# Performance work log

Measured on AMD Instinct MI355X. Metric: run time of the kernel, lower is better.

The kernel has to match this reference:

```python
import jax, jax.numpy as jnp
import numpy as np

EPS = 1e-5


def conv1x1(x, w, b):
    # x: [B,C,H,W], w: [O,C], b: [O]
    return jnp.einsum('bchw,oc->bohw', x, w) + b[None, :, None, None]


def adain(content, style):
    # Standard AdaIN: instance-normalize content, re-scale with style's
    # per-channel instance statistics.
    mu_c = content.mean(axis=(2, 3), keepdims=True)
    std_c = jnp.sqrt(content.var(axis=(2, 3), keepdims=True) + EPS)
    mu_s = style.mean(axis=(2, 3), keepdims=True)
    std_s = jnp.sqrt(style.var(axis=(2, 3), keepdims=True) + EPS)
    return std_s * (content - mu_c) / std_c + mu_s


def setup_inputs() -> dict:
    key = jax.random.key(0)
    ks = jax.random.split(key, 12)
    B, C, H, W = 4, 512, 64, 64
    C8 = C // 8
    s_in = 1.0 / np.sqrt(C)
    s_mid = 1.0 / np.sqrt(C8)
    return {
        'x0': jax.random.normal(ks[0], (B, C, H, W), jnp.float32),
        'x1': jax.random.normal(ks[1], (B, C, H, W), jnp.float32),
        'g_w': jax.random.normal(ks[2], (C8, C), jnp.float32) * s_in,
        'g_b': jnp.zeros((C8,), jnp.float32),
        'theta_w': jax.random.normal(ks[3], (C8, C), jnp.float32) * s_in,
        'theta_b': jnp.zeros((C8,), jnp.float32),
        'phi_w': jax.random.normal(ks[4], (C8, C), jnp.float32) * s_in,
        'phi_b': jnp.zeros((C8,), jnp.float32),
        'W_w': jax.random.normal(ks[5], (C, C8), jnp.float32) * s_mid,
        'W_b': jnp.zeros((C,), jnp.float32),
    }


def reference(x0, x1, g_w, g_b, theta_w, theta_b, phi_w, phi_b, W_w, W_b):
    B, C, H, W = x0.shape
    N = H * W
    C8 = C // 8
    g_x = conv1x1(x0, g_w, g_b).reshape(B, C8, N).transpose(0, 2, 1)      # [B,N,C8]
    theta_x = conv1x1(x1, theta_w, theta_b).reshape(B, C8, N)             # [B,C8,N]
    phi_x = conv1x1(x1, phi_w, phi_b).reshape(B, C8, N).transpose(0, 2, 1)  # [B,N,C8]
    f = jnp.einsum('bnc,bcm->bnm', phi_x, theta_x)                        # [B,N,N]
    f_div_C = jax.nn.softmax(f, axis=-1)
    y = jnp.einsum('bnm,bmc->bnc', f_div_C, g_x)                          # [B,N,C8]
    # Faithful to torch .view: reinterpret contiguous [B,N,C8] as [B,C8,H,W]
    y = y.reshape(B, C8, H, W)
    W_y = conv1x1(y, W_w, W_b)                                            # [B,C,H,W]
    return adain(x0, W_y)
```

## Files before the change

kernel.cpp:

```cpp
#include <hip/hip_runtime.h>

#define BB 4
#define CC 512
#define C8 64
#define NN 4096
#define EPSI 1e-5f

typedef unsigned short ushort_t;
typedef unsigned int uint;
typedef __bf16 bf16x8 __attribute__((ext_vector_type(8)));
typedef float f32x4 __attribute__((ext_vector_type(4)));

__device__ inline ushort_t f2bf(float f) {
  uint u = __float_as_uint(f);
  uint r = (u + 0x7FFFu + ((u >> 16) & 1u)) >> 16;
  return (ushort_t)r;
}

__device__ inline bf16x8 ld_bf8(const ushort_t* p) {
  uint4 u = *(const uint4*)p;
  return __builtin_bit_cast(bf16x8, u);
}

__global__ __launch_bounds__(256) void wconv_kernel(
    const float* __restrict__ tw, const float* __restrict__ pw,
    const float* __restrict__ gw, ushort_t* __restrict__ twb,
    ushort_t* __restrict__ pwb, ushort_t* __restrict__ gwb) {
  const int sec = blockIdx.x >> 5;
  const int idx = ((blockIdx.x & 31) * 256 + threadIdx.x) * 4;
  const float* src = sec == 0 ? tw : (sec == 1 ? pw : gw);
  ushort_t* dst = sec == 0 ? twb : (sec == 1 ? pwb : gwb);
  float4 v = *(const float4*)(src + idx);
  uint2 pk;
  pk.x = (uint)f2bf(v.x) | ((uint)f2bf(v.y) << 16);
  pk.y = (uint)f2bf(v.z) | ((uint)f2bf(v.w) << 16);
  *(uint2*)(dst + idx) = pk;
}

__global__ __launch_bounds__(256) void proj2_mfma_kernel(
    const float* __restrict__ x1,
    const ushort_t* __restrict__ twb, const float* __restrict__ tb,
    const ushort_t* __restrict__ pwb, const float* __restrict__ pb,
    ushort_t* __restrict__ thetaT, ushort_t* __restrict__ phiT) {
  __shared__ char xT[32 * 128];
  const int b = blockIdx.y;
  const int n0 = blockIdx.x * 32;
  const int t = threadIdx.x;
  const int l = t & 63;
  const int w = t >> 6;
  const int l15 = l & 15;
  const int lg = l >> 4;
  const int ns = w & 1;
  const int isphi = w >> 1;
  const float* xb = x1 + (size_t)b * CC * NN;
  const ushort_t* wb = isphi ? pwb : twb;
  const float* bias = isphi ? pb : tb;
  ushort_t* outp = isphi ? phiT : thetaT;

  f32x4 acc[4];
#pragma unroll
  for (int s = 0; s < 4; ++s) acc[s] = {0.f, 0.f, 0.f, 0.f};

  const int ldrow = t >> 3;
  const int ldc4 = t & 7;
  const int nfr = ns * 16 + l15;
  const int fchunkbase = nfr * 128;
  for (int k0 = 0; k0 < CC; k0 += 64) {
    __syncthreads();
#pragma unroll
    for (int p = 0; p < 2; ++p) {
      const int kr = ldrow + p * 32;
      float4 v = *(const float4*)(xb + (size_t)(k0 + kr) * NN + n0 + ldc4 * 4);
      ushort_t e0 = f2bf(v.x), e1 = f2bf(v.y), e2 = f2bf(v.z), e3 = f2bf(v.w);
      const int chunk = kr >> 3;
      const int kin = (kr & 7) * 2;
#pragma unroll
      for (int j = 0; j < 4; ++j) {
        const int n = ldc4 * 4 + j;
        ushort_t e = j == 0 ? e0 : (j == 1 ? e1 : (j == 2 ? e2 : e3));
        *(ushort_t*)(xT + n * 128 + (((chunk ^ (n & 7)) << 4) | kin)) = e;
      }
    }
    __syncthreads();
#pragma unroll
    for (int ks = 0; ks < 2; ++ks) {
      bf16x8 bx = *(const bf16x8*)(xT + fchunkbase +
                                   (((ks * 4 + lg) ^ (nfr & 7)) << 4));
#pragma unroll
      for (int rs = 0; rs < 4; ++rs) {
        bf16x8 aw = ld_bf8(wb + (size_t)(rs * 16 + l15) * 512 + k0 + ks * 32 + lg * 8);
        acc[rs] = __builtin_amdgcn_mfma_f32_16x16x32_bf16(aw, bx, acc[rs], 0, 0, 0);
      }
    }
  }
  const size_t nrow = (size_t)b * NN + n0 + ns * 16 + l15;
#pragma unroll
  for (int rs = 0; rs < 4; ++rs) {
    float4 bv = *(const float4*)(bias + rs * 16 + lg * 4);
    float a0 = acc[rs][0] + bv.x;
    float a1 = acc[rs][1] + bv.y;
    float a2 = acc[rs][2] + bv.z;
    float a3 = acc[rs][3] + bv.w;
    uint d0, d1;
    asm("v_cvt_pk_bf16_f32 %0, %1, %2" : "=v"(d0) : "v"(a0), "v"(a1));
    asm("v_cvt_pk_bf16_f32 %0, %1, %2" : "=v"(d1) : "v"(a2), "v"(a3));
    uint2 pk; pk.x = d0; pk.y = d1;
    *(uint2*)(outp + nrow * 64 + rs * 16 + lg * 4) = pk;
  }
}

__global__ __launch_bounds__(256) void proj1_mfma_kernel(
    const float* __restrict__ x0,
    const ushort_t* __restrict__ gwb, const float* __restrict__ gbias,
    ushort_t* __restrict__ g) {
  __shared__ char xT[32 * 128];
  const int b = blockIdx.y;
  const int n0 = blockIdx.x * 32;
  const int t = threadIdx.x;
  const int l = t & 63;
  const int w = t >> 6;
  const int l15 = l & 15;
  const int lg = l >> 4;
  const int ns = w & 1;
  const int rh = w >> 1;
  const float* xb = x0 + (size_t)b * CC * NN;

  f32x4 acc[2];
#pragma unroll
  for (int s = 0; s < 2; ++s) acc[s] = {0.f, 0.f, 0.f, 0.f};

  const int ldrow = t >> 3;
  const int ldc4 = t & 7;
  const int nfr = ns * 16 + l15;
  const int fchunkbase = nfr * 128;
  for (int k0 = 0; k0 < CC; k0 += 64) {
    __syncthreads();
#pragma unroll
    for (int p = 0; p < 2; ++p) {
      const int kr = ldrow + p * 32;
      float4 v = *(const float4*)(xb + (size_t)(k0 + kr) * NN + n0 + ldc4 * 4);
      ushort_t e0 = f2bf(v.x), e1 = f2bf(v.y), e2 = f2bf(v.z), e3 = f2bf(v.w);
      const int chunk = kr >> 3;
      const int kin = (kr & 7) * 2;
#pragma unroll
      for (int j = 0; j < 4; ++j) {
        const int n = ldc4 * 4 + j;
        ushort_t e = j == 0 ? e0 : (j == 1 ? e1 : (j == 2 ? e2 : e3));
        *(ushort_t*)(xT + n * 128 + (((chunk ^ (n & 7)) << 4) | kin)) = e;
      }
    }
    __syncthreads();
#pragma unroll
    for (int ks = 0; ks < 2; ++ks) {
      bf16x8 bx = *(const bf16x8*)(xT + fchunkbase +
                                   (((ks * 4 + lg) ^ (nfr & 7)) << 4));
#pragma unroll
      for (int j = 0; j < 2; ++j) {
        const int rs = rh * 2 + j;
        bf16x8 aw = ld_bf8(gwb + (size_t)(rs * 16 + l15) * 512 + k0 + ks * 32 + lg * 8);
        acc[j] = __builtin_amdgcn_mfma_f32_16x16x32_bf16(aw, bx, acc[j], 0, 0, 0);
      }
    }
  }
  const int ncol = n0 + ns * 16 + l15;
#pragma unroll
  for (int j = 0; j < 2; ++j) {
    const int rbase = (rh * 2 + j) * 16 + lg * 4;
    float4 bv = *(const float4*)(gbias + rbase);
    g[((size_t)b * 64 + rbase + 0) * NN + ncol] = f2bf(acc[j][0] + bv.x);
    g[((size_t)b * 64 + rbase + 1) * NN + ncol] = f2bf(acc[j][1] + bv.y);
    g[((size_t)b * 64 + rbase + 2) * NN + ncol] = f2bf(acc[j][2] + bv.z);
    g[((size_t)b * 64 + rbase + 3) * NN + ncol] = f2bf(acc[j][3] + bv.w);
  }
}

__global__ __launch_bounds__(128) void attn_mfma_kernel(
    const ushort_t* __restrict__ thT,
    const ushort_t* __restrict__ phT,
    const ushort_t* __restrict__ gm,
    float* __restrict__ y) {
  __shared__ char Plds[2][2048];
  const int b = blockIdx.y;
  const int q0 = blockIdx.x * 32;
  const int tid = threadIdx.x;
  const int l = tid & 63;
  const int w = tid >> 6;
  const int l15 = l & 15;
  const int lg = l >> 4;
  const ushort_t* thB = thT + (size_t)b * NN * 64;
  const ushort_t* phB = phT + (size_t)b * NN * 64;
  const ushort_t* gB = gm + (size_t)b * 64 * NN;
  char* Pw = Plds[w];

  bf16x8 qf[2];
  {
    const ushort_t* p = phB + (size_t)(q0 + w * 16 + l15) * 64 + lg * 8;
    qf[0] = ld_bf8(p);
    qf[1] = ld_bf8(p + 32);
  }

  float m_run = -1e30f, l_run = 0.f;
  f32x4 acc[4];
#pragma unroll
  for (int s = 0; s < 4; ++s) acc[s] = {0.f, 0.f, 0.f, 0.f};

  const ushort_t* thL = thB + (size_t)l15 * 64 + lg * 8;
  const ushort_t* gL = gB + (size_t)l15 * 4096 + lg * 8;
  const int pwr = l15 * 128;
  const uint pswz = (uint)((l & 7) << 4);

  for (int m0 = 0; m0 < NN; m0 += 64) {
    f32x4 st[4];
#pragma unroll
    for (int s = 0; s < 4; ++s) st[s] = {0.f, 0.f, 0.f, 0.f};
#pragma unroll
    for (int s = 0; s < 4; ++s) {
      const ushort_t* ts = thL + (size_t)(m0 + 16 * s) * 64;
      bf16x8 a0 = ld_bf8(ts);
      bf16x8 a1 = ld_bf8(ts + 32);
      st[s] = __builtin_amdgcn_mfma_f32_16x16x32_bf16(a0, qf[0], st[s], 0, 0, 0);
      st[s] = __builtin_amdgcn_mfma_f32_16x16x32_bf16(a1, qf[1], st[s], 0, 0, 0);
    }
    bf16x8 ga[4][2];
#pragma unroll
    for (int s = 0; s < 4; ++s) {
      const ushort_t* gs = gL + (size_t)s * 16 * 4096 + m0;
      ga[s][0] = ld_bf8(gs);
      ga[s][1] = ld_bf8(gs + 32);
    }
    float tmax = -1e30f;
#pragma unroll
    for (int s = 0; s < 4; ++s)
#pragma unroll
      for (int r = 0; r < 4; ++r) tmax = fmaxf(tmax, st[s][r]);
    tmax = fmaxf(tmax, __shfl_xor(tmax, 16));
    tmax = fmaxf(tmax, __shfl_xor(tmax, 32));
    const float mn = fmaxf(m_run, tmax);
    const float sc = __expf(m_run - mn);
    float tsum = 0.f;
#pragma unroll
    for (int s = 0; s < 4; ++s)
#pragma unroll
      for (int r = 0; r < 4; ++r) {
        float p = __expf(st[s][r] - mn);
        st[s][r] = p;
        tsum += p;
      }
    tsum += __shfl_xor(tsum, 16);
    tsum += __shfl_xor(tsum, 32);
    l_run = l_run * sc + tsum;
    m_run = mn;
#pragma unroll
    for (int s = 0; s < 4; ++s) acc[s] *= sc;
#pragma unroll
    for (int s = 0; s < 4; ++s) {
      uint d0, d1;
      float a0 = st[s][0], a1 = st[s][1], a2 = st[s][2], a3 = st[s][3];
      asm("v_cvt_pk_bf16_f32 %0, %1, %2" : "=v"(d0) : "v"(a0), "v"(a1));
      asm("v_cvt_pk_bf16_f32 %0, %1, %2" : "=v"(d1) : "v"(a2), "v"(a3));
      const uint mb = (uint)((16 * s + lg * 4) * 2);
      char* wp = Pw + pwr + (int)((mb & 15u) | ((mb & ~15u) ^ pswz));
      unsigned long long v = (unsigned long long)d0 | ((unsigned long long)d1 << 32);
      *(unsigned long long*)wp = v;
    }
#pragma unroll
    for (int k = 0; k < 2; ++k) {
      const uint rb = (uint)(lg * 16 + 64 * k);
      bf16x8 pbf = ld_bf8((const ushort_t*)(Pw + pwr + (int)(rb ^ pswz)));
#pragma unroll
      for (int s = 0; s < 4; ++s)
        acc[s] = __builtin_amdgcn_mfma_f32_16x16x32_bf16(ga[s][k], pbf, acc[s], 0, 0, 0);
    }
  }
  const float inv = 1.f / l_run;
  float* yB = y + ((size_t)b * NN + q0 + w * 16 + l15) * 64;
#pragma unroll
  for (int s = 0; s < 4; ++s) {
    float4 o;
    o.x = acc[s][0] * inv;
    o.y = acc[s][1] * inv;
    o.z = acc[s][2] * inv;
    o.w = acc[s][3] * inv;
    *(float4*)(yB + 16 * s + lg * 4) = o;
  }
}

__global__ void zero_kernel(float* __restrict__ p, int n) {
  int i = blockIdx.x * blockDim.x + threadIdx.x;
  if (i < n) p[i] = 0.f;
}

__global__ __launch_bounds__(256) void gram_kernel(const float* __restrict__ y,
                                                   float* __restrict__ Gm) {
  __shared__ float ys[64][65];
  const int b = blockIdx.y;
  const int m0 = blockIdx.x * 64;
  const int t = threadIdx.x;
  const float* yb = y + (size_t)b * (NN * C8);
#pragma unroll
  for (int j = 0; j < 16; ++j) {
    int k = (t >> 6) + j * 4;
    ys[k][t & 63] = yb[(size_t)k * NN + m0 + (t & 63)];
  }
  __syncthreads();
  const int k = t >> 2;
  const int k2b = (t & 3) * 16;
  float a_[16];
#pragma unroll
  for (int i = 0; i < 16; ++i) a_[i] = 0.f;
  for (int m = 0; m < 64; ++m) {
    float av = ys[k][m];
#pragma unroll
    for (int i = 0; i < 16; ++i) a_[i] += av * ys[k2b + i][m];
  }
#pragma unroll
  for (int i = 0; i < 16; ++i)
    atomicAdd(&Gm[(size_t)b * 4096 + k * 64 + k2b + i], a_[i]);
}

__global__ __launch_bounds__(64) void ybar_kernel(const float* __restrict__ y,
                                                  float* __restrict__ yb) {
  const int k = blockIdx.x, b = blockIdx.y, l = threadIdx.x;
  const float* row = y + (size_t)b * (NN * C8) + (size_t)k * NN;
  float s = 0.f;
  for (int j = l; j < NN; j += 64) s += row[j];
#pragma unroll
  for (int off = 32; off >= 1; off >>= 1) s += __shfl_xor(s, off);
  if (l == 0) yb[b * 64 + k] = s * (1.f / NN);
}

__global__ __launch_bounds__(64) void wy_stats_kernel(
    const float* __restrict__ Gm, const float* __restrict__ ybar,
    const float* __restrict__ Ww, const float* __restrict__ Wb,
    float* __restrict__ mu_s, float* __restrict__ std_s) {
  __shared__ float ww[64];
  const int o = blockIdx.x, b = blockIdx.y, l = threadIdx.x;
  ww[l] = Ww[o * 64 + l];
  __syncthreads();
  const float* Gb = Gm + (size_t)b * 4096;
  float colsum = 0.f;
  for (int k = 0; k < 64; ++k) colsum += ww[k] * Gb[k * 64 + l];
  float qq = ww[l] * colsum;
  float md = ww[l] * ybar[b * 64 + l];
#pragma unroll
  for (int off = 32; off >= 1; off >>= 1) {
    qq += __shfl_xor(qq, off);
    md += __shfl_xor(md, off);
  }
  if (l == 0) {
    float bias = Wb[o];
    float mu = md + bias;
    float ex2 = qq * (1.f / NN) + 2.f * bias * md + bias * bias;
    float var = ex2 - mu * mu;
    mu_s[b * CC + o] = mu;
    std_s[b * CC + o] = sqrtf(fmaxf(var, 0.f) + EPSI);
  }
}

__global__ __launch_bounds__(256) void x_stats_kernel(const float* __restrict__ x0,
                                                      float* __restrict__ mu_c,
                                                      float* __restrict__ rstd_c) {
  __shared__ float redA[4], redB[4];
  const int c = blockIdx.x, b = blockIdx.y, t = threadIdx.x;
  const float4* xi = (const float4*)(x0 + ((size_t)b * CC + c) * NN);
  float s1 = 0.f, s2 = 0.f;
#pragma unroll
  for (int j = t; j < NN / 4; j += 256) {
    float4 v = xi[j];
    s1 += v.x + v.y + v.z + v.w;
    s2 += v.x * v.x + v.y * v.y + v.z * v.z + v.w * v.w;
  }
#pragma unroll
  for (int off = 32; off >= 1; off >>= 1) {
    s1 += __shfl_xor(s1, off);
    s2 += __shfl_xor(s2, off);
  }
  if ((t & 63) == 0) { redA[t >> 6] = s1; redB[t >> 6] = s2; }
  __syncthreads();
  if (t == 0) {
    float S1 = redA[0] + redA[1] + redA[2] + redA[3];
    float S2 = redB[0] + redB[1] + redB[2] + redB[3];
    float mean = S1 * (1.f / NN);
    float var = S2 * (1.f / NN) - mean * mean;
    mu_c[b * CC + c] = mean;
    rstd_c[b * CC + c] = 1.f / sqrtf(var + EPSI);
  }
}

__global__ __launch_bounds__(256) void adain_kernel(
    const float* __restrict__ x0, const float* __restrict__ mu_c,
    const float* __restrict__ rstd_c, const float* __restrict__ mu_s,
    const float* __restrict__ std_s, float* __restrict__ out) {
  const int c = blockIdx.x, b = blockIdx.y, t = threadIdx.x;
  const int bc = b * CC + c;
  const float scale = std_s[bc] * rstd_c[bc];
  const float shift = mu_s[bc] - scale * mu_c[bc];
  const float4* xi = (const float4*)(x0 + (size_t)bc * NN);
  float4* oo = (float4*)(out + (size_t)bc * NN);
#pragma unroll
  for (int j = t; j < NN / 4; j += 256) {
    float4 v = xi[j];
    v.x = v.x * scale + shift;
    v.y = v.y * scale + shift;
    v.z = v.z * scale + shift;
    v.w = v.w * scale + shift;
    oo[j] = v;
  }
}

extern "C" void kernel_launch(void* const* d_in, const int* in_sizes, int n_in,
                              void* d_out, int out_size, void* d_ws, size_t ws_size,
                              hipStream_t stream) {
  (void)in_sizes; (void)n_in; (void)out_size; (void)ws_size;
  const float* x0 = (const float*)d_in[0];
  const float* x1 = (const float*)d_in[1];
  const float* g_w = (const float*)d_in[2];
  const float* g_b = (const float*)d_in[3];
  const float* theta_w = (const float*)d_in[4];
  const float* theta_b = (const float*)d_in[5];
  const float* phi_w = (const float*)d_in[6];
  const float* phi_b = (const float*)d_in[7];
  const float* W_w = (const float*)d_in[8];
  const float* W_b = (const float*)d_in[9];
  float* out = (float*)d_out;
  float* ws = (float*)d_ws;

  ushort_t* thetaT = (ushort_t*)ws;
  ushort_t* phiT = (ushort_t*)(ws + 524288);
  ushort_t* gbf = (ushort_t*)(ws + 1048576);
  float* y = ws + 1572864;
  float* Gm = ws + 2621440;
  float* yb = ws + 2637824;
  float* mu_s = ws + 2638080;
  float* std_s = ws + 2640128;
  float* mu_c = ws + 2642176;
  float* rstd_c = ws + 2644224;
  ushort_t* twb = (ushort_t*)(ws + 2646272);
  ushort_t* pwb = (ushort_t*)(ws + 2662656);
  ushort_t* gwb = (ushort_t*)(ws + 2679040);

  wconv_kernel<<<dim3(96), 256, 0, stream>>>(theta_w, phi_w, g_w, twb, pwb, gwb);
  proj2_mfma_kernel<<<dim3(128, BB), 256, 0, stream>>>(x1, twb, theta_b, pwb,
                                                       phi_b, thetaT, phiT);
  proj1_mfma_kernel<<<dim3(128, BB), 256, 0, stream>>>(x0, gwb, g_b, gbf);
  attn_mfma_kernel<<<dim3(128, BB), 128, 0, stream>>>(thetaT, phiT, gbf, y);
  zero_kernel<<<dim3(64), 256, 0, stream>>>(Gm, BB * 64 * 64);
  gram_kernel<<<dim3(64, BB), 256, 0, stream>>>(y, Gm);
  ybar_kernel<<<dim3(64, BB), 64, 0, stream>>>(y, yb);
  wy_stats_kernel<<<dim3(CC, BB), 64, 0, stream>>>(Gm, yb, W_w, W_b, mu_s, std_s);
  x_stats_kernel<<<dim3(CC, BB), 256, 0, stream>>>(x0, mu_c, rstd_c);
  adain_kernel<<<dim3(CC, BB), 256, 0, stream>>>(x0, mu_c, rstd_c, mu_s, std_s, out);
}
```

Before: 355.6 us.

## Split attention key range across four waves and merge partial softmax in LDS

```diff
diff --git a/kernel.cpp b/kernel.cpp
--- a/kernel.cpp
+++ b/kernel.cpp
@@ -174,12 +174,14 @@
   }
 }
 
-__global__ __launch_bounds__(128) void attn_mfma_kernel(
+__global__ __launch_bounds__(256) void attn_mfma_kernel(
     const ushort_t* __restrict__ thT,
     const ushort_t* __restrict__ phT,
     const ushort_t* __restrict__ gm,
     float* __restrict__ y) {
-  __shared__ char Plds[2][2048];
+  __shared__ char Plds[4][2][2048];
+  __shared__ float pacc[4][32][64];
+  __shared__ float pm[4][32], pl[4][32];
   const int b = blockIdx.y;
   const int q0 = blockIdx.x * 32;
   const int tid = threadIdx.x;
@@ -190,36 +192,43 @@
   const ushort_t* thB = thT + (size_t)b * NN * 64;
   const ushort_t* phB = phT + (size_t)b * NN * 64;
   const ushort_t* gB = gm + (size_t)b * 64 * NN;
-  char* Pw = Plds[w];
-
-  bf16x8 qf[2];
-  {
-    const ushort_t* p = phB + (size_t)(q0 + w * 16 + l15) * 64 + lg * 8;
-    qf[0] = ld_bf8(p);
-    qf[1] = ld_bf8(p + 32);
-  }
-
-  float m_run = -1e30f, l_run = 0.f;
-  f32x4 acc[4];
-#pragma unroll
-  for (int s = 0; s < 4; ++s) acc[s] = {0.f, 0.f, 0.f, 0.f};
+
+  bf16x8 qf[2][2];
+#pragma unroll
+  for (int qg = 0; qg < 2; ++qg) {
+    const ushort_t* p = phB + (size_t)(q0 + qg * 16 + l15) * 64 + lg * 8;
+    qf[qg][0] = ld_bf8(p);
+    qf[qg][1] = ld_bf8(p + 32);
+  }
+
+  float m_run[2] = {-1e30f, -1e30f}, l_run[2] = {0.f, 0.f};
+  f32x4 acc[2][4];
+#pragma unroll
+  for (int qg = 0; qg < 2; ++qg)
+#pragma unroll
+    for (int s = 0; s < 4; ++s) acc[qg][s] = {0.f, 0.f, 0.f, 0.f};
 
   const ushort_t* thL = thB + (size_t)l15 * 64 + lg * 8;
   const ushort_t* gL = gB + (size_t)l15 * 4096 + lg * 8;
   const int pwr = l15 * 128;
   const uint pswz = (uint)((l & 7) << 4);
-
-  for (int m0 = 0; m0 < NN; m0 += 64) {
-    f32x4 st[4];
-#pragma unroll
-    for (int s = 0; s < 4; ++s) st[s] = {0.f, 0.f, 0.f, 0.f};
+  const int mbeg = w * (NN / 4);
+
+  for (int m0 = mbeg; m0 < mbeg + NN / 4; m0 += 64) {
+    f32x4 st[2][4];
+#pragma unroll
+    for (int qg = 0; qg < 2; ++qg)
+#pragma unroll
+      for (int s = 0; s < 4; ++s) st[qg][s] = {0.f, 0.f, 0.f, 0.f};
 #pragma unroll
     for (int s = 0; s < 4; ++s) {
       const ushort_t* ts = thL + (size_t)(m0 + 16 * s) * 64;
       bf16x8 a0 = ld_bf8(ts);
       bf16x8 a1 = ld_bf8(ts + 32);
-      st[s] = __builtin_amdgcn_mfma_f32_16x16x32_bf16(a0, qf[0], st[s], 0, 0, 0);
-      st[s] = __builtin_amdgcn_mfma_f32_16x16x32_bf16(a1, qf[1], st[s], 0, 0, 0);
+      st[0][s] = __builtin_amdgcn_mfma_f32_16x16x32_bf16(a0, qf[0][0], st[0][s], 0, 0, 0);
+      st[1][s] = __builtin_amdgcn_mfma_f32_16x16x32_bf16(a0, qf[1][0], st[1][s], 0, 0, 0);
+      st[0][s] = __builtin_amdgcn_mfma_f32_16x16x32_bf16(a1, qf[0][1], st[0][s], 0, 0, 0);
+      st[1][s] = __builtin_amdgcn_mfma_f32_16x16x32_bf16(a1, qf[1][1], st[1][s], 0, 0, 0);
     }
     bf16x8 ga[4][2];
 #pragma unroll
@@ -228,60 +237,93 @@
       ga[s][0] = ld_bf8(gs);
       ga[s][1] = ld_bf8(gs + 32);
     }
-    float tmax = -1e30f;
+#pragma unroll
+    for (int qg = 0; qg < 2; ++qg) {
+      float tmax = -1e30f;
+#pragma unroll
+      for (int s = 0; s < 4; ++s)
+#pragma unroll
+        for (int r = 0; r < 4; ++r) tmax = fmaxf(tmax, st[qg][s][r]);
+      tmax = fmaxf(tmax, __shfl_xor(tmax, 16));
+      tmax = fmaxf(tmax, __shfl_xor(tmax, 32));
+      const float mn = fmaxf(m_run[qg], tmax);
+      const float sc = __expf(m_run[qg] - mn);
+      float tsum = 0.f;
+#pragma unroll
+      for (int s = 0; s < 4; ++s)
+#pragma unroll
+        for (int r = 0; r < 4; ++r) {
+          float p = __expf(st[qg][s][r] - mn);
+          st[qg][s][r] = p;
+          tsum += p;
+        }
+      tsum += __shfl_xor(tsum, 16);
+      tsum += __shfl_xor(tsum, 32);
+      l_run[qg] = l_run[qg] * sc + tsum;
+      m_run[qg] = mn;
+#pragma unroll
+      for (int s = 0; s < 4; ++s) acc[qg][s] *= sc;
+      char* Pw = Plds[w][qg];
+#pragma unroll
+      for (int s = 0; s < 4; ++s) {
+        uint d0, d1;
+        float a0 = st[qg][s][0], a1 = st[qg][s][1], a2 = st[qg][s][2], a3 = st[qg][s][3];
+        asm("v_cvt_pk_bf16_f32 %0, %1, %2" : "=v"(d0) : "v"(a0), "v"(a1));
+        asm("v_cvt_pk_bf16_f32 %0, %1, %2" : "=v"(d1) : "v"(a2), "v"(a3));
+        const uint mb = (uint)((16 * s + lg * 4) * 2);
+        char* wp = Pw + pwr + (int)((mb & 15u) | ((mb & ~15u) ^ pswz));
+        unsigned long long v = (unsigned long long)d0 | ((unsigned long long)d1 << 32);
+        *(unsigned long long*)wp = v;
+      }
+    }
+#pragma unroll
+    for (int qg = 0; qg < 2; ++qg) {
+      char* Pw = Plds[w][qg];
+#pragma unroll
+      for (int k = 0; k < 2; ++k) {
+        const uint rb = (uint)(lg * 16 + 64 * k);
+        bf16x8 pbf = ld_bf8((const ushort_t*)(Pw + pwr + (int)(rb ^ pswz)));
+#pragma unroll
+        for (int s = 0; s < 4; ++s)
+          acc[qg][s] = __builtin_amdgcn_mfma_f32_16x16x32_bf16(ga[s][k], pbf, acc[qg][s], 0, 0, 0);
+      }
+    }
+  }
+#pragma unroll
+  for (int qg = 0; qg < 2; ++qg) {
+    const int q = qg * 16 + l15;
 #pragma unroll
     for (int s = 0; s < 4; ++s)
-#pragma unroll
-      for (int r = 0; r < 4; ++r) tmax = fmaxf(tmax, st[s][r]);
-    tmax = fmaxf(tmax, __shfl_xor(tmax, 16));
-    tmax = fmaxf(tmax, __shfl_xor(tmax, 32));
-    const float mn = fmaxf(m_run, tmax);
-    const float sc = __expf(m_run - mn);
-    float tsum = 0.f;
-#pragma unroll
-    for (int s = 0; s < 4; ++s)
-#pragma unroll
-      for (int r = 0; r < 4; ++r) {
-        float p = __expf(st[s][r] - mn);
-        st[s][r] = p;
-        tsum += p;
-      }
-    tsum += __shfl_xor(tsum, 16);
-    tsum += __shfl_xor(tsum, 32);
-    l_run = l_run * sc + tsum;
-    m_run = mn;
-#pragma unroll
-    for (int s = 0; s < 4; ++s) acc[s] *= sc;
-#pragma unroll
-    for (int s = 0; s < 4; ++s) {
-      uint d0, d1;
-      float a0 = st[s][0], a1 = st[s][1], a2 = st[s][2], a3 = st[s][3];
-      asm("v_cvt_pk_bf16_f32 %0, %1, %2" : "=v"(d0) : "v"(a0), "v"(a1));
-      asm("v_cvt_pk_bf16_f32 %0, %1, %2" : "=v"(d1) : "v"(a2), "v"(a3));
-      const uint mb = (uint)((16 * s + lg * 4) * 2);
-      char* wp = Pw + pwr + (int)((mb & 15u) | ((mb & ~15u) ^ pswz));
-      unsigned long long v = (unsigned long long)d0 | ((unsigned long long)d1 << 32);
-      *(unsigned long long*)wp = v;
-    }
-#pragma unroll
-    for (int k = 0; k < 2; ++k) {
-      const uint rb = (uint)(lg * 16 + 64 * k);
-      bf16x8 pbf = ld_bf8((const ushort_t*)(Pw + pwr + (int)(rb ^ pswz)));
-#pragma unroll
-      for (int s = 0; s < 4; ++s)
-        acc[s] = __builtin_amdgcn_mfma_f32_16x16x32_bf16(ga[s][k], pbf, acc[s], 0, 0, 0);
-    }
-  }
-  const float inv = 1.f / l_run;
-  float* yB = y + ((size_t)b * NN + q0 + w * 16 + l15) * 64;
-#pragma unroll
-  for (int s = 0; s < 4; ++s) {
-    float4 o;
-    o.x = acc[s][0] * inv;
-    o.y = acc[s][1] * inv;
-    o.z = acc[s][2] * inv;
-    o.w = acc[s][3] * inv;
-    *(float4*)(yB + 16 * s + lg * 4) = o;
+      *(f32x4*)&pacc[w][q][16 * s + lg * 4] = acc[qg][s];
+    if (lg == 0) {
+      pm[w][q] = m_run[qg];
+      pl[w][q] = l_run[qg];
+    }
+  }
+  __syncthreads();
+  {
+    const int q = tid >> 3;
+    const int cb = (tid & 7) * 8;
+    float m0v = pm[0][q], m1v = pm[1][q], m2v = pm[2][q], m3v = pm[3][q];
+    float M = fmaxf(fmaxf(m0v, m1v), fmaxf(m2v, m3v));
+    float e0 = __expf(m0v - M), e1 = __expf(m1v - M);
+    float e2 = __expf(m2v - M), e3 = __expf(m3v - M);
+    float L = pl[0][q] * e0 + pl[1][q] * e1 + pl[2][q] * e2 + pl[3][q] * e3;
+    float inv = 1.f / L;
+    float* yB = y + ((size_t)b * NN + q0 + q) * 64 + cb;
+#pragma unroll
+    for (int h = 0; h < 2; ++h) {
+      float4 o;
+      o.x = (pacc[0][q][cb + 4 * h + 0] * e0 + pacc[1][q][cb + 4 * h + 0] * e1 +
+             pacc[2][q][cb + 4 * h + 0] * e2 + pacc[3][q][cb + 4 * h + 0] * e3) * inv;
+      o.y = (pacc[0][q][cb + 4 * h + 1] * e0 + pacc[1][q][cb + 4 * h + 1] * e1 +
+             pacc[2][q][cb + 4 * h + 1] * e2 + pacc[3][q][cb + 4 * h + 1] * e3) * inv;
+      o.z = (pacc[0][q][cb + 4 * h + 2] * e0 + pacc[1][q][cb + 4 * h + 2] * e1 +
+             pacc[2][q][cb + 4 * h + 2] * e2 + pacc[3][q][cb + 4 * h + 2] * e3) * inv;
+      o.w = (pacc[0][q][cb + 4 * h + 3] * e0 + pacc[1][q][cb + 4 * h + 3] * e1 +
+             pacc[2][q][cb + 4 * h + 3] * e2 + pacc[3][q][cb + 4 * h + 3] * e3) * inv;
+      *(float4*)(yB + 4 * h) = o;
+    }
   }
 }
 
@@ -443,7 +485,7 @@
   proj2_mfma_kernel<<<dim3(128, BB), 256, 0, stream>>>(x1, twb, theta_b, pwb,
                                                        phi_b, thetaT, phiT);
   proj1_mfma_kernel<<<dim3(128, BB), 256, 0, stream>>>(x0, gwb, g_b, gbf);
-  attn_mfma_kernel<<<dim3(128, BB), 128, 0, stream>>>(thetaT, phiT, gbf, y);
+  attn_mfma_kernel<<<dim3(128, BB), 256, 0, stream>>>(thetaT, phiT, gbf, y);
   zero_kernel<<<dim3(64), 256, 0, stream>>>(Gm, BB * 64 * 64);
   gram_kernel<<<dim3(64, BB), 256, 0, stream>>>(y, Gm);
   ybar_kernel<<<dim3(64, BB), 64, 0, stream>>>(y, yb);
```

Result: faster. 302.6 us (-14.9%).
